# Kernel optimization log

Measured on AMD Instinct MI355X. Metric: run time of the kernel, lower is better.

The kernel has to match this reference:

```python
import jax, jax.numpy as jnp
import numpy as np

NEG_SLOPE = 0.2

def gat_layer(x, src, dst, W, al, ar, b):
    # x: (N, F_in); W: (F_in, H*D); al/ar: (H, D); b: (H, D)
    N = x.shape[0]
    H, D = al.shape
    feat = (x @ W).reshape(N, H, D)                      # (N,H,D)
    el = jnp.sum(feat * al, axis=-1)                     # (N,H) src-side scores
    er = jnp.sum(feat * ar, axis=-1)                     # (N,H) dst-side scores
    e = jax.nn.leaky_relu(el[src] + er[dst], NEG_SLOPE)  # (E,H)
    # edge softmax over incoming edges of each dst node (numerically stable)
    m = jax.ops.segment_max(e, dst, num_segments=N)      # (N,H)
    m = jnp.where(jnp.isfinite(m), m, 0.0)               # guard isolated nodes
    ex = jnp.exp(e - m[dst])                             # (E,H)
    denom = jax.ops.segment_sum(ex, dst, num_segments=N) # (N,H)
    alpha = ex / jnp.maximum(denom[dst], 1e-30)          # (E,H)
    msg = alpha[:, :, None] * feat[src]                  # (E,H,D) gather + weight
    out = jax.ops.segment_sum(msg, dst, num_segments=N)  # (N,H,D) scatter-add
    return out + b[None]                                 # bias per head


def setup_inputs() -> dict:
    key = jax.random.key(0)
    ks = jax.random.split(key, 12)
    N, E, F_in, Dh = 100000, 1600000, 128, 64
    H1 = 2
    inp = {}
    inp['in_feat'] = jax.random.normal(ks[0], (N, F_in), dtype=jnp.float32)
    inp['src'] = jax.random.randint(ks[1], (E,), 0, N, dtype=jnp.int32)
    inp['dst'] = jax.random.randint(ks[2], (E,), 0, N, dtype=jnp.int32)
    s1 = 1.0 / np.sqrt(F_in)
    inp['W1'] = jax.random.normal(ks[3], (F_in, H1 * Dh), dtype=jnp.float32) * s1
    inp['al1'] = jax.random.normal(ks[4], (H1, Dh), dtype=jnp.float32) * 0.1
    inp['ar1'] = jax.random.normal(ks[5], (H1, Dh), dtype=jnp.float32) * 0.1
    inp['b1'] = jnp.zeros((H1, Dh), dtype=jnp.float32)
    s2 = 1.0 / np.sqrt(Dh)
    inp['W2'] = jax.random.normal(ks[6], (Dh, 1 * 2), dtype=jnp.float32) * s2
    inp['al2'] = jax.random.normal(ks[7], (1, 2), dtype=jnp.float32) * 0.1
    inp['ar2'] = jax.random.normal(ks[8], (1, 2), dtype=jnp.float32) * 0.1
    inp['b2'] = jnp.zeros((1, 2), dtype=jnp.float32)
    return inp


def reference(in_feat, src, dst, W1, al1, ar1, b1, W2, al2, ar2, b2):
    num_heads = al1.shape[0]
    h = gat_layer(in_feat, src, dst, W1, al1, ar1, b1)  # (N,2,64)
    h = jnp.sum(h, axis=1) / num_heads                  # head mean
    h = jax.nn.relu(h)
    out = gat_layer(h, src, dst, W2, al2, ar2, b2)      # (N,1,2)
    return out
```

## Files before the change

### kernel.cpp

```cpp
#include <hip/hip_runtime.h>
#include <hip/hip_bf16.h>
#include <hip/hip_fp16.h>

#define LEAKY 0.2f
#define NBMAX 1024
#define CCH   4096
#define SCAP2 3456

typedef _Float16 half8 __attribute__((ext_vector_type(8)));
typedef float f32x4 __attribute__((ext_vector_type(4)));

__device__ __forceinline__ float wave_sum64(float v) {
    #pragma unroll
    for (int m = 32; m > 0; m >>= 1) v += __shfl_xor(v, m, 64);
    return v;
}

__launch_bounds__(256)
__global__ void prep_kernel(const float* __restrict__ W, __half* __restrict__ Wt,
                            const int* __restrict__ dst, int* __restrict__ bcount,
                            int E, int NB) {
    __shared__ int hls[NBMAX];
    for (int i = threadIdx.x; i < NB; i += 256) hls[i] = 0;
    __syncthreads();
    if (blockIdx.x < 64) {
        int i = blockIdx.x * 256 + threadIdx.x;
        int n = i >> 7, k = i & 127;
        Wt[i] = __float2half(W[k * 128 + n]);
    }
    int stride = gridDim.x * 256;
    for (int e = blockIdx.x * 256 + threadIdx.x; e < E; e += stride)
        atomicAdd(&hls[dst[e] >> 7], 1);
    __syncthreads();
    for (int i = threadIdx.x; i < NB; i += 256) {
        int c = hls[i];
        if (c) atomicAdd(&bcount[i], c);
    }
}

__launch_bounds__(256)
__global__ void gemm1_kernel(const float* __restrict__ X, const __half* __restrict__ Wt,
                             const float* __restrict__ al1, const float* __restrict__ ar1,
                             unsigned char* __restrict__ feat8, __half* __restrict__ sch,
                             float* __restrict__ el1, float* __restrict__ er1, int N) {
    __shared__ __half Al[64 * 136];
    __shared__ __half Wl[128 * 136];
    const int tid = threadIdx.x;
    const int r0 = blockIdx.x * 64;
    {
        int n = tid >> 1, h0 = (tid & 1) * 64;
        const __half* gsrc = Wt + n * 128 + h0;
        __half* ldst = Wl + n * 136 + h0;
        #pragma unroll
        for (int i = 0; i < 8; i++)
            *(uint4*)(ldst + i * 8) = *(const uint4*)(gsrc + i * 8);
    }
    {
        int r = tid >> 2, c0 = (tid & 3) * 32;
        int rr = r0 + r;
        const float* gsrc = X + (size_t)rr * 128 + c0;
        __half* ldst = Al + r * 136 + c0;
        if (rr < N) {
            #pragma unroll
            for (int i = 0; i < 8; i++) {
                float4 v = *(const float4*)(gsrc + i * 4);
                __half2 a = __floats2half2_rn(v.x, v.y);
                __half2 b = __floats2half2_rn(v.z, v.w);
                uint2 pk; pk.x = *(unsigned*)&a; pk.y = *(unsigned*)&b;
                *(uint2*)(ldst + i * 4) = pk;
            }
        } else {
            uint2 z; z.x = 0; z.y = 0;
            #pragma unroll
            for (int i = 0; i < 8; i++) *(uint2*)(ldst + i * 4) = z;
        }
    }
    __syncthreads();
    const int wv = tid >> 6, lane = tid & 63;
    const int lm = lane & 15, lq = lane >> 4;
    f32x4 acc[8];
    #pragma unroll
    for (int t = 0; t < 8; t++) acc[t] = (f32x4){0.f, 0.f, 0.f, 0.f};
    const __half* arow = Al + (wv * 16 + lm) * 136 + lq * 8;
    const __half* brow = Wl + lm * 136 + lq * 8;
    #pragma unroll
    for (int ks = 0; ks < 4; ks++) {
        half8 af = *(const half8*)(arow + ks * 32);
        #pragma unroll
        for (int nt = 0; nt < 8; nt++) {
            half8 bf = *(const half8*)(brow + nt * 16 * 136 + ks * 32);
            acc[nt] = __builtin_amdgcn_mfma_f32_16x16x32_f16(af, bf, acc[nt], 0, 0, 0);
        }
    }
    __syncthreads();
    __half* Cl = Al;
    #pragma unroll
    for (int nt = 0; nt < 8; nt++) {
        #pragma unroll
        for (int r = 0; r < 4; r++) {
            int m = wv * 16 + lq * 4 + r;
            Cl[m * 136 + nt * 16 + lm] = __float2half(acc[nt][r]);
        }
    }
    __syncthreads();
    {
        int r = tid >> 2, c0 = (tid & 3) * 32;
        int rr = r0 + r;
        float pel = 0.f, per = 0.f;
        const __half* crow = Cl + r * 136 + c0;
        if (rr < N) {
            float am = 0.f;
            #pragma unroll
            for (int c = 0; c < 32; c++) {
                float fv = __half2float(crow[c]);
                pel += fv * al1[c0 + c];
                per += fv * ar1[c0 + c];
                am = fmaxf(am, fabsf(fv));
            }
            am = fmaxf(am, __shfl_xor(am, 1, 64));
            am = fmaxf(am, __shfl_xor(am, 2, 64));
            float s = __half2float(__float2half_rn(fmaxf(am, 1e-8f) * (1.f / 127.5f)));
            float is = 1.f / s;
            unsigned pk8[8];
            #pragma unroll
            for (int i = 0; i < 8; i++) {
                unsigned w = 0;
                #pragma unroll
                for (int k = 0; k < 4; k++) {
                    float fv = __half2float(crow[i * 4 + k]);
                    int q = (int)rintf(fv * is + 127.5f);
                    q = q < 0 ? 0 : (q > 255 ? 255 : q);
                    w |= (unsigned)q << (8 * k);
                }
                pk8[i] = w;
            }
            *(uint4*)(feat8 + (size_t)rr * 128 + c0) = *(const uint4*)&pk8[0];
            *(uint4*)(feat8 + (size_t)rr * 128 + c0 + 16) = *(const uint4*)&pk8[4];
            if ((tid & 3) == 0) sch[rr] = __float2half_rn(s);
        }
        pel += __shfl_xor(pel, 1, 64);
        per += __shfl_xor(per, 1, 64);
        if ((tid & 1) == 0 && rr < N) {
            int h = (tid >> 1) & 1;
            el1[rr * 2 + h] = pel;
            er1[rr * 2 + h] = per;
        }
    }
}

__launch_bounds__(1024)
__global__ void bscan_kernel(const int* __restrict__ bcount, int* __restrict__ bstart,
                             int* __restrict__ bcursor, int NB) {
    __shared__ int sd[NBMAX];
    int t = threadIdx.x;
    int v = (t < NB) ? bcount[t] : 0;
    sd[t] = v;
    __syncthreads();
    for (int o = 1; o < NBMAX; o <<= 1) {
        int x = (t >= o) ? sd[t - o] : 0;
        __syncthreads();
        sd[t] += x;
        __syncthreads();
    }
    if (t < NB) { int ex = sd[t] - v; bstart[t] = ex; bcursor[t] = ex; }
}

__launch_bounds__(256)
__global__ void bscatter_kernel(const int* __restrict__ src, const int* __restrict__ dst,
                                const float* __restrict__ el1, const float* __restrict__ er1,
                                int* __restrict__ bcursor, uint2* __restrict__ erec,
                                int E, int NB) {
    __shared__ int hls[NBMAX];
    for (int i = threadIdx.x; i < NB; i += 256) hls[i] = 0;
    __syncthreads();
    const int b0 = blockIdx.x * CCH;
    uint2 ureg[16];
    int breg[16];
    #pragma unroll
    for (int k = 0; k < 16; k++) {
        int e = b0 + k * 256 + threadIdx.x;
        if (e < E) {
            int s = src[e], d = dst[e];
            int bk = d >> 7;
            breg[k] = bk;
            float2 lv = *((const float2*)el1 + s);
            float2 rv = *((const float2*)er1 + d);
            float e0 = lv.x + rv.x; e0 = (e0 > 0.f) ? e0 : LEAKY * e0;
            float e1 = lv.y + rv.y; e1 = (e1 > 0.f) ? e1 : LEAKY * e1;
            __half2 w = __floats2half2_rn(__expf(e0), __expf(e1));
            ureg[k].x = ((unsigned)s << 7) | (unsigned)(d & 127);
            ureg[k].y = *(unsigned*)&w;
            atomicAdd(&hls[bk], 1);
        } else breg[k] = -1;
    }
    __syncthreads();
    for (int b = threadIdx.x; b < NB; b += 256) {
        int c = hls[b];
        if (c) hls[b] = atomicAdd(&bcursor[b], c);
    }
    __syncthreads();
    #pragma unroll
    for (int k = 0; k < 16; k++) {
        if (breg[k] >= 0) {
            int p = atomicAdd(&hls[breg[k]], 1);
            erec[p] = ureg[k];
        }
    }
}

__launch_bounds__(256)
__global__ void bsort_kernel(const uint2* __restrict__ erec,
                             const int* __restrict__ bstart, const int* __restrict__ bcount,
                             uint2* __restrict__ erec2,
                             int* __restrict__ rowstart, int* __restrict__ plen,
                             int* __restrict__ tlen,
                             int N, int NB) {
    __shared__ uint2 sorted[SCAP2];
    __shared__ int cnt[128], prs[129], curs[128];
    const int tid = threadIdx.x;
    const int b = blockIdx.x;
    const int node0 = b << 7;
    const int nd = min(128, N - node0);
    const int ebase = bstart[b];
    int ecnt = bcount[b];
    if (ecnt > SCAP2 - 896) ecnt = SCAP2 - 896;
    const int pbase = ebase + 896 * b;
    if (tid < 128) cnt[tid] = 0;
    __syncthreads();
    for (int j = tid; j < ecnt; j += 256)
        atomicAdd(&cnt[erec[ebase + j].x & 127], 1);
    __syncthreads();
    int pv = 0;
    if (tid < 128) { pv = (cnt[tid] + 7) & ~7; curs[tid] = pv; }
    __syncthreads();
    for (int o = 1; o < 128; o <<= 1) {
        int x = 0;
        if (tid < 128 && tid >= o) x = curs[tid - o];
        __syncthreads();
        if (tid < 128) curs[tid] += x;
        __syncthreads();
    }
    if (tid < 128) prs[tid + 1] = curs[tid];
    if (tid == 0) prs[0] = 0;
    __syncthreads();
    if (tid < 128) curs[tid] = prs[tid + 1] - pv;
    __syncthreads();
    const int pecnt = prs[128];
    for (int j = tid; j < pecnt; j += 256) { sorted[j].x = 0; sorted[j].y = 0; }
    __syncthreads();
    for (int j = tid; j < ecnt; j += 256) {
        uint2 r = erec[ebase + j];
        int p = atomicAdd(&curs[r.x & 127], 1);
        uint2 o2;
        o2.x = (r.x >> 7) << 8;
        o2.y = r.y;
        sorted[p] = o2;
    }
    __syncthreads();
    for (int j = tid; j < pecnt; j += 256) erec2[(size_t)pbase + j] = sorted[j];
    if (tid < nd) {
        rowstart[node0 + tid] = pbase + prs[tid];
        plen[node0 + tid] = prs[tid + 1] - prs[tid];
        tlen[node0 + tid] = cnt[tid];
    }
}

__device__ __forceinline__ void acc_edge16(uint2 r, uint2 v, unsigned short sh, unsigned hsh,
                                           float* acc, float& den, float& csum) {
    float w = __half2float(__ushort_as_half((unsigned short)((r.y >> hsh) & 0xffffu)));
    den += w;
    float s = __half2float(__ushort_as_half(sh));
    float a = w * s;
    csum += a;
    acc[0] += a * (float)(v.x & 0xffu);
    acc[1] += a * (float)((v.x >> 8) & 0xffu);
    acc[2] += a * (float)((v.x >> 16) & 0xffu);
    acc[3] += a * (float)(v.x >> 24);
    acc[4] += a * (float)(v.y & 0xffu);
    acc[5] += a * (float)((v.y >> 8) & 0xffu);
    acc[6] += a * (float)((v.y >> 16) & 0xffu);
    acc[7] += a * (float)(v.y >> 24);
}

__launch_bounds__(256)
__global__ void agg1_kernel(const char* __restrict__ fh, const __half* __restrict__ sch,
                            const uint2* __restrict__ erec2,
                            const float* __restrict__ b1, const float* __restrict__ W2,
                            const float* __restrict__ ar2,
                            const int* __restrict__ rowstart, const int* __restrict__ plen,
                            float* __restrict__ feat2, float* __restrict__ er2, int N) {
    int node = (blockIdx.x * 256 + threadIdx.x) >> 4;
    int l4 = threadIdx.x & 15;
    if (node >= N) return;
    const int len = plen[node];
    const uint2* __restrict__ rp = erec2 + rowstart[node];
    const unsigned hsh = (l4 < 8) ? 0u : 16u;
    const unsigned lofs = (unsigned)l4 * 8u;
    float acc[8];
    #pragma unroll
    for (int k = 0; k < 8; k++) acc[k] = 0.f;
    float den = 0.f, csum = 0.f;

#define LDR(R, g) do { const uint2* _p = rp + (g) * 4;                             \
        R[0] = _p[0]; R[1] = _p[1]; R[2] = _p[2]; R[3] = _p[3]; } while (0)
#define GTH(V, S, R) do {                                                          \
        V[0] = *(const uint2*)(fh + ((R[0].x >> 1) + lofs));                       \
        V[1] = *(const uint2*)(fh + ((R[1].x >> 1) + lofs));                       \
        V[2] = *(const uint2*)(fh + ((R[2].x >> 1) + lofs));                       \
        V[3] = *(const uint2*)(fh + ((R[3].x >> 1) + lofs));                       \
        S[0] = *(const unsigned short*)(sch + (R[0].x >> 8));                      \
        S[1] = *(const unsigned short*)(sch + (R[1].x >> 8));                      \
        S[2] = *(const unsigned short*)(sch + (R[2].x >> 8));                      \
        S[3] = *(const unsigned short*)(sch + (R[3].x >> 8)); } while (0)
#define ACC(R, V, S) do {                                                          \
        acc_edge16(R[0], V[0], S[0], hsh, acc, den, csum);                         \
        acc_edge16(R[1], V[1], S[1], hsh, acc, den, csum);                         \
        acc_edge16(R[2], V[2], S[2], hsh, acc, den, csum);                         \
        acc_edge16(R[3], V[3], S[3], hsh, acc, den, csum); } while (0)

    const int n4 = len >> 2;
    if (n4 > 0) {
        uint2 ra[4], rb[4], va[4], vb[4];
        unsigned short sa[4], sb[4];
        LDR(ra, 0);
        if (n4 > 1) LDR(rb, 1);
        GTH(va, sa, ra);
        int g = 0;
        while (g + 1 < n4) {
            GTH(vb, sb, rb);
            ACC(ra, va, sa);
            if (g + 2 < n4) LDR(ra, g + 2);
            g++;
            if (g + 1 >= n4) { ACC(rb, vb, sb); g++; break; }
            GTH(va, sa, ra);
            ACC(rb, vb, sb);
            if (g + 2 < n4) LDR(rb, g + 2);
            g++;
        }
        if (g < n4) ACC(ra, va, sa);
    }
#undef LDR
#undef GTH
#undef ACC

    const float corr = 127.5f * csum;
    const float inv = 1.f / fmaxf(den, 1e-30f);
    const float* browp = b1 + l4 * 8;
    float4 bb0 = *(const float4*)browp;
    float4 bb1 = *(const float4*)(browp + 4);
    float o[8];
    o[0] = (acc[0] - corr) * inv + bb0.x;
    o[1] = (acc[1] - corr) * inv + bb0.y;
    o[2] = (acc[2] - corr) * inv + bb0.z;
    o[3] = (acc[3] - corr) * inv + bb0.w;
    o[4] = (acc[4] - corr) * inv + bb1.x;
    o[5] = (acc[5] - corr) * inv + bb1.y;
    o[6] = (acc[6] - corr) * inv + bb1.z;
    o[7] = (acc[7] - corr) * inv + bb1.w;
    float m[8];
    #pragma unroll
    for (int k = 0; k < 8; k++) {
        float t = o[k] + __shfl_xor(o[k], 8, 64);
        m[k] = fmaxf(0.5f * t, 0.f);
    }
    const float* wrow = W2 + (l4 & 7) * 16;
    float p0 = 0.f, p1 = 0.f;
    #pragma unroll
    for (int k = 0; k < 8; k++) {
        p0 += m[k] * wrow[k * 2 + 0];
        p1 += m[k] * wrow[k * 2 + 1];
    }
    p0 += __shfl_xor(p0, 4, 64); p0 += __shfl_xor(p0, 2, 64); p0 += __shfl_xor(p0, 1, 64);
    p1 += __shfl_xor(p1, 4, 64); p1 += __shfl_xor(p1, 2, 64); p1 += __shfl_xor(p1, 1, 64);
    if (l4 == 0) {
        float2 f2; f2.x = p0; f2.y = p1;
        *((float2*)feat2 + node) = f2;
        er2[node] = p0 * ar2[0] + p1 * ar2[1];
    }
}

__launch_bounds__(256)
__global__ void agg2_kernel(const float* __restrict__ feat2, const float* __restrict__ er2,
                            const float* __restrict__ al2, const float* __restrict__ b2,
                            const int* __restrict__ rowstart, const int* __restrict__ tlen,
                            const uint2* __restrict__ erec2, float* __restrict__ out, int N) {
    int node = (blockIdx.x * 256 + threadIdx.x) >> 4;
    int l4 = threadIdx.x & 15;
    if (node >= N) return;
    const int len = tlen[node];
    const uint2* rp = erec2 + rowstart[node];
    const float ern = er2[node];
    const float al20 = al2[0], al21 = al2[1];
    float den = 0.f, a0 = 0.f, a1 = 0.f;
    for (int j = l4; j < len; j += 16) {
        unsigned key = rp[j].x;
        float2 f = *((const float2*)feat2 + (key >> 8));
        float e = f.x * al20 + f.y * al21 + ern;
        e = (e > 0.f) ? e : LEAKY * e;
        float w = __expf(e);
        den += w;
        a0 += w * f.x;
        a1 += w * f.y;
    }
    #pragma unroll
    for (int m = 1; m < 16; m <<= 1) {
        den += __shfl_xor(den, m, 64);
        a0  += __shfl_xor(a0, m, 64);
        a1  += __shfl_xor(a1, m, 64);
    }
    if (l4 == 0) {
        float inv = 1.f / fmaxf(den, 1e-30f);
        float2 o;
        o.x = a0 * inv + b2[0];
        o.y = a1 * inv + b2[1];
        *((float2*)out + node) = o;
    }
}

extern "C" void kernel_launch(void* const* d_in, const int* in_sizes, int n_in,
                              void* d_out, int out_size, void* d_ws, size_t ws_size,
                              hipStream_t stream) {
    const float* in_feat = (const float*)d_in[0];
    const int*   src     = (const int*)d_in[1];
    const int*   dst     = (const int*)d_in[2];
    const float* W1      = (const float*)d_in[3];
    const float* al1     = (const float*)d_in[4];
    const float* ar1     = (const float*)d_in[5];
    const float* b1      = (const float*)d_in[6];
    const float* W2      = (const float*)d_in[7];
    const float* al2     = (const float*)d_in[8];
    const float* ar2     = (const float*)d_in[9];
    const float* b2      = (const float*)d_in[10];
    float* out = (float*)d_out;

    const int N = in_sizes[0] / 128;
    const int E = in_sizes[1];
    const int NB = (N + 127) >> 7;

    char* ws = (char*)d_ws;
    unsigned char* feat8 = (unsigned char*)ws;
    size_t off = (size_t)N * 128;
    __half* scaleh = (__half*)(ws + off); off += (size_t)N * 2;
    float* el1 = (float*)(ws + off); off += (size_t)N * 2 * 4;
    float* er1 = (float*)(ws + off); off += (size_t)N * 2 * 4;
    float* feat2 = (float*)(ws + off); off += (size_t)N * 2 * 4;
    float* er2 = (float*)(ws + off); off += (size_t)N * 4;
    int* bcount  = (int*)(ws + off); off += NBMAX * 4;
    int* bstart  = (int*)(ws + off); off += NBMAX * 4;
    int* bcursor = (int*)(ws + off); off += NBMAX * 4;
    int* rowstart = (int*)(ws + off); off += (size_t)N * 4;
    int* plen     = (int*)(ws + off); off += (size_t)N * 4;
    int* tlen     = (int*)(ws + off); off += (size_t)N * 4;
    uint2* erec  = (uint2*)(ws + off); off += (size_t)E * 8;
    uint2* erec2 = (uint2*)(ws + off); off += ((size_t)E + 896 * NB) * 8;
    __half* W1t = (__half*)(ws + off); off += 128 * 128 * 2;
    (void)ws_size; (void)n_in; (void)out_size;

    hipMemsetAsync(bcount, 0, NBMAX * 4, stream);

    const int nblkC = (E + CCH - 1) / CCH;
    prep_kernel<<<nblkC, 256, 0, stream>>>(W1, W1t, dst, bcount, E, NB);
    gemm1_kernel<<<(N + 63) / 64, 256, 0, stream>>>(in_feat, W1t, al1, ar1,
                                                    feat8, scaleh, el1, er1, N);

    bscan_kernel<<<1, 1024, 0, stream>>>(bcount, bstart, bcursor, NB);
    bscatter_kernel<<<nblkC, 256, 0, stream>>>(src, dst, el1, er1, bcursor, erec, E, NB);
    bsort_kernel<<<NB, 256, 0, stream>>>(erec, bstart, bcount, erec2, rowstart, plen, tlen, N, NB);

    agg1_kernel<<<(N * 16 + 255) / 256, 256, 0, stream>>>(
        (const char*)feat8, scaleh, erec2, b1, W2, ar2, rowstart, plen, feat2, er2, N);

    agg2_kernel<<<(N * 16 + 255) / 256, 256, 0, stream>>>(
        feat2, er2, al2, b2, rowstart, tlen, erec2, out, N);
}
```

Baseline: 249.3 us.

## Fold bucket scan into prep kernel via last-block pattern, widen blocks

The separate single-block scan kernel is removed. The last block of prep_kernel to finish, detected through an atomic done counter and a threadfence, now computes the exclusive scan of the bucket counts and writes bstart and bcursor. prep and bscatter now run 512-thread blocks over 8192-edge chunks, which halves the block count and the global atomics on bucket counters. This saves one kernel launch, but the scan now sits on the tail of prep, and bscatter's larger blocks raise register pressure from the 16-entry per-thread arrays.

```diff
diff --git a/kernel.cpp b/kernel.cpp
--- a/kernel.cpp
+++ b/kernel.cpp
@@ -4,7 +4,7 @@
 
 #define LEAKY 0.2f
 #define NBMAX 1024
-#define CCH   4096
+#define CCH   8192
 #define SCAP2 3456
 
 typedef _Float16 half8 __attribute__((ext_vector_type(8)));
@@ -16,26 +16,49 @@
     return v;
 }
 
-__launch_bounds__(256)
+__launch_bounds__(512)
 __global__ void prep_kernel(const float* __restrict__ W, __half* __restrict__ Wt,
                             const int* __restrict__ dst, int* __restrict__ bcount,
-                            int E, int NB) {
+                            int* __restrict__ bstart, int* __restrict__ bcursor,
+                            int* __restrict__ donec, int E, int NB) {
     __shared__ int hls[NBMAX];
-    for (int i = threadIdx.x; i < NB; i += 256) hls[i] = 0;
-    __syncthreads();
-    if (blockIdx.x < 64) {
-        int i = blockIdx.x * 256 + threadIdx.x;
+    for (int i = threadIdx.x; i < NB; i += 512) hls[i] = 0;
+    __syncthreads();
+    if (blockIdx.x < 32) {
+        int i = blockIdx.x * 512 + threadIdx.x;
         int n = i >> 7, k = i & 127;
         Wt[i] = __float2half(W[k * 128 + n]);
     }
-    int stride = gridDim.x * 256;
-    for (int e = blockIdx.x * 256 + threadIdx.x; e < E; e += stride)
+    int stride = gridDim.x * 512;
+    for (int e = blockIdx.x * 512 + threadIdx.x; e < E; e += stride)
         atomicAdd(&hls[dst[e] >> 7], 1);
     __syncthreads();
-    for (int i = threadIdx.x; i < NB; i += 256) {
+    for (int i = threadIdx.x; i < NB; i += 512) {
         int c = hls[i];
         if (c) atomicAdd(&bcount[i], c);
     }
+    __threadfence();
+    __shared__ int lastFlag;
+    if (threadIdx.x == 0)
+        lastFlag = (atomicAdd(donec, 1) == (int)gridDim.x - 1) ? 1 : 0;
+    __syncthreads();
+    if (!lastFlag) return;
+    __shared__ int sd[NBMAX];
+    const int t = threadIdx.x;
+    volatile int* vb = bcount;
+    int v0 = (t < NB) ? vb[t] : 0;
+    int v1 = (t + 512 < NB) ? vb[t + 512] : 0;
+    sd[t] = v0; sd[t + 512] = v1;
+    __syncthreads();
+    for (int o = 1; o < NBMAX; o <<= 1) {
+        int x0 = (t >= o) ? sd[t - o] : 0;
+        int x1 = sd[t + 512 - o];
+        __syncthreads();
+        sd[t] += x0; sd[t + 512] += x1;
+        __syncthreads();
+    }
+    if (t < NB)       { int ex = sd[t] - v0;       bstart[t] = ex;       bcursor[t] = ex; }
+    if (t + 512 < NB) { int ex = sd[t + 512] - v1; bstart[t + 512] = ex; bcursor[t + 512] = ex; }
 }
 
 __launch_bounds__(256)
@@ -148,37 +171,20 @@
     }
 }
 
-__launch_bounds__(1024)
-__global__ void bscan_kernel(const int* __restrict__ bcount, int* __restrict__ bstart,
-                             int* __restrict__ bcursor, int NB) {
-    __shared__ int sd[NBMAX];
-    int t = threadIdx.x;
-    int v = (t < NB) ? bcount[t] : 0;
-    sd[t] = v;
-    __syncthreads();
-    for (int o = 1; o < NBMAX; o <<= 1) {
-        int x = (t >= o) ? sd[t - o] : 0;
-        __syncthreads();
-        sd[t] += x;
-        __syncthreads();
-    }
-    if (t < NB) { int ex = sd[t] - v; bstart[t] = ex; bcursor[t] = ex; }
-}
-
-__launch_bounds__(256)
+__launch_bounds__(512)
 __global__ void bscatter_kernel(const int* __restrict__ src, const int* __restrict__ dst,
                                 const float* __restrict__ el1, const float* __restrict__ er1,
                                 int* __restrict__ bcursor, uint2* __restrict__ erec,
                                 int E, int NB) {
     __shared__ int hls[NBMAX];
-    for (int i = threadIdx.x; i < NB; i += 256) hls[i] = 0;
+    for (int i = threadIdx.x; i < NB; i += 512) hls[i] = 0;
     __syncthreads();
     const int b0 = blockIdx.x * CCH;
     uint2 ureg[16];
     int breg[16];
     #pragma unroll
     for (int k = 0; k < 16; k++) {
-        int e = b0 + k * 256 + threadIdx.x;
+        int e = b0 + k * 512 + threadIdx.x;
         if (e < E) {
             int s = src[e], d = dst[e];
             int bk = d >> 7;
@@ -194,7 +200,7 @@
         } else breg[k] = -1;
     }
     __syncthreads();
-    for (int b = threadIdx.x; b < NB; b += 256) {
+    for (int b = threadIdx.x; b < NB; b += 512) {
         int c = hls[b];
         if (c) hls[b] = atomicAdd(&bcursor[b], c);
     }
@@ -446,6 +452,7 @@
     float* feat2 = (float*)(ws + off); off += (size_t)N * 2 * 4;
     float* er2 = (float*)(ws + off); off += (size_t)N * 4;
     int* bcount  = (int*)(ws + off); off += NBMAX * 4;
+    int* donec   = (int*)(ws + off); off += 16;
     int* bstart  = (int*)(ws + off); off += NBMAX * 4;
     int* bcursor = (int*)(ws + off); off += NBMAX * 4;
     int* rowstart = (int*)(ws + off); off += (size_t)N * 4;
@@ -456,15 +463,14 @@
     __half* W1t = (__half*)(ws + off); off += 128 * 128 * 2;
     (void)ws_size; (void)n_in; (void)out_size;
 
-    hipMemsetAsync(bcount, 0, NBMAX * 4, stream);
+    hipMemsetAsync(bcount, 0, NBMAX * 4 + 16, stream);
 
     const int nblkC = (E + CCH - 1) / CCH;
-    prep_kernel<<<nblkC, 256, 0, stream>>>(W1, W1t, dst, bcount, E, NB);
+    prep_kernel<<<nblkC, 512, 0, stream>>>(W1, W1t, dst, bcount, bstart, bcursor,
+                                           donec, E, NB);
     gemm1_kernel<<<(N + 63) / 64, 256, 0, stream>>>(in_feat, W1t, al1, ar1,
                                                     feat8, scaleh, el1, er1, N);
-
-    bscan_kernel<<<1, 1024, 0, stream>>>(bcount, bstart, bcursor, NB);
-    bscatter_kernel<<<nblkC, 256, 0, stream>>>(src, dst, el1, er1, bcursor, erec, E, NB);
+    bscatter_kernel<<<nblkC, 512, 0, stream>>>(src, dst, el1, er1, bcursor, erec, E, NB);
     bsort_kernel<<<NB, 256, 0, stream>>>(erec, bstart, bcount, erec2, rowstart, plen, tlen, N, NB);
 
     agg1_kernel<<<(N * 16 + 255) / 256, 256, 0, stream>>>(
```

Result: slower. 263.9 us (+5.9%).
